# Performance work log

Hardware: AMD Instinct MI355X
Metric: run time of the kernel (lower is better)

## Reference

```python
import jax, jax.numpy as jnp
import numpy as np

B, N, D = 16, 2048, 1024
DEPTH, H, DH = 6, 16, 64
INNER = H * DH          # 1024
NL = 64                 # num latents
FF = 4 * D              # 4096
OUT = 1024


def _ln(x, g, b):
    m = jnp.mean(x, axis=-1, keepdims=True)
    v = jnp.mean((x - m) ** 2, axis=-1, keepdims=True)
    return (x - m) * jax.lax.rsqrt(v + 1e-5) * g + b


def setup_inputs() -> dict:
    key = jax.random.key(0)
    ks = jax.random.split(key, 10)
    s = lambda k, shape: (jax.random.normal(k, shape) * 0.02).astype(jnp.float32)
    return dict(
        embeds=jax.random.normal(ks[0], (B, N, D), dtype=jnp.float32),
        latents=jax.random.normal(ks[1], (NL, D), dtype=jnp.float32),
        Wq=s(ks[2], (DEPTH, D, INNER)),
        Wkv=s(ks[3], (DEPTH, D, 2 * INNER)),
        Wo=s(ks[4], (DEPTH, INNER, D)),
        W1=s(ks[5], (DEPTH, D, FF)),
        W2=s(ks[6], (DEPTH, FF, D)),
        ln_media_g=jnp.ones((DEPTH, D)), ln_media_b=jnp.zeros((DEPTH, D)),
        ln_lat_g=jnp.ones((DEPTH, D)), ln_lat_b=jnp.zeros((DEPTH, D)),
        ff_ln_g=jnp.ones((DEPTH, D)), ff_ln_b=jnp.zeros((DEPTH, D)),
        proj_W=s(ks[7], (D, OUT)),
        proj_b=jnp.zeros((OUT,)),
        final_g=jnp.ones((OUT,)), final_b=jnp.zeros((OUT,)),
        mask=jax.random.randint(ks[8], (B, N), 0, 2).astype(jnp.int32),
    )


def reference(embeds, latents, Wq, Wkv, Wo, W1, W2,
              ln_media_g, ln_media_b, ln_lat_g, ln_lat_b,
              ff_ln_g, ff_ln_b, proj_W, proj_b, final_g, final_b, mask):
    b = embeds.shape[0]
    scale = DH ** -0.5
    # cat latent mask of ones, then broadcast over (head, query) dims
    full_mask = jnp.concatenate(
        [mask.astype(embeds.dtype), jnp.ones((b, NL), embeds.dtype)], axis=1)
    keep = full_mask[:, None, None, :] > 0          # (b, 1, 1, N+NL)
    lat = jnp.broadcast_to(latents[None], (b, NL, D))
    for i in range(DEPTH):
        # --- masked cross-attention ---
        x = _ln(embeds, ln_media_g[i], ln_media_b[i])
        l = _ln(lat, ln_lat_g[i], ln_lat_b[i])
        q = (l @ Wq[i]).reshape(b, NL, H, DH).transpose(0, 2, 1, 3) * scale
        kv = jnp.concatenate([x, l], axis=1) @ Wkv[i]     # (b, N+NL, 2*inner)
        k, v = jnp.split(kv, 2, axis=-1)
        k = k.reshape(b, -1, H, DH).transpose(0, 2, 1, 3)
        v = v.reshape(b, -1, H, DH).transpose(0, 2, 1, 3)
        sim = jnp.einsum('bhid,bhjd->bhij', q, k)
        sim = sim - jax.lax.stop_gradient(jnp.max(sim, axis=-1, keepdims=True))
        sim = jnp.where(keep, sim, -10000.0)
        attn = jax.nn.softmax(sim, axis=-1)
        o = jnp.einsum('bhij,bhjd->bhid', attn, v)
        o = o.transpose(0, 2, 1, 3).reshape(b, NL, INNER)
        lat = o @ Wo[i] + lat
        # --- feed-forward ---
        h = _ln(lat, ff_ln_g[i], ff_ln_b[i])
        lat = jax.nn.gelu(h @ W1[i], approximate=False) @ W2[i] + lat
    out = lat @ proj_W + proj_b
    return _ln(out, final_g, final_b)
```

## Files before the change

kernel.cpp:

```cpp
#include <hip/hip_runtime.h>
#include <cstdint>
#include <cstddef>

typedef __bf16 bf16x8 __attribute__((ext_vector_type(8)));
typedef float f32x4 __attribute__((ext_vector_type(4)));
typedef int i32x4 __attribute__((ext_vector_type(4)));
typedef unsigned short u16;
typedef unsigned short u16x4 __attribute__((ext_vector_type(4)));

#define DEVI __device__ __forceinline__

namespace {

constexpr int kB = 16;
constexpr int kN = 2048;
constexpr int kD = 1024;
constexpr int kDepth = 6;
constexpr int kH = 16;
constexpr int kInner = 1024;
constexpr int kNL = 64;
constexpr int kFF = 4096;
constexpr int kTok = kN + kNL;

constexpr int EPI_BF16 = 0, EPI_KV_X = 1, EPI_KV_L = 2, EPI_RES = 3,
              EPI_RES_BF = 4, EPI_GELU = 5, EPI_BIAS = 6;

DEVI u16 f2bf(float f) {
  unsigned u = __builtin_bit_cast(unsigned, f);
  return (u16)((u + 0x7fffu + ((u >> 16) & 1u)) >> 16);
}
DEVI float bf2f(u16 u) { return __builtin_bit_cast(float, (unsigned)u << 16); }

__global__ __launch_bounds__(256)
void compact_k(const int* __restrict__ mask, int* __restrict__ pos,
               int* __restrict__ cnt, int* __restrict__ cpad)
{
  const int b = blockIdx.x;
  const int tid = threadIdx.x;
  __shared__ int warp_tot[4];
  const int* mb = mask + (size_t)b * kN;
  int v[8]; int loc = 0;
  #pragma unroll
  for (int j = 0; j < 8; ++j) { v[j] = (mb[tid * 8 + j] != 0); loc += v[j]; }
  int pre = loc;
  #pragma unroll
  for (int off = 1; off < 64; off <<= 1) {
    int t = __shfl_up(pre, off);
    if ((tid & 63) >= off) pre += t;
  }
  if ((tid & 63) == 63) warp_tot[tid >> 6] = pre;
  __syncthreads();
  int wbase = 0;
  for (int w = 0; w < (tid >> 6); ++w) wbase += warp_tot[w];
  const int total = warp_tot[0] + warp_tot[1] + warp_tot[2] + warp_tot[3];
  int idx = wbase + pre - loc;
  int* pb = pos + (size_t)b * kN;
  #pragma unroll
  for (int j = 0; j < 8; ++j)
    if (v[j]) pb[idx++] = tid * 8 + j;
  if (tid == 0) { cnt[b] = total; cpad[b] = (total + 127) & ~127; }
}

template<bool OBF>
__global__ __launch_bounds__(256)
void ln_k(const float* __restrict__ in, const float* __restrict__ g,
          const float* __restrict__ b, void* __restrict__ out)
{
  const int row = blockIdx.x;
  const int tid = threadIdx.x;
  const f32x4 v = *(const f32x4*)(in + (size_t)row * kD + tid * 4);
  float s = v[0] + v[1] + v[2] + v[3];
  float ss = v[0]*v[0] + v[1]*v[1] + v[2]*v[2] + v[3]*v[3];
  #pragma unroll
  for (int off = 1; off < 64; off <<= 1) {
    s += __shfl_xor(s, off);
    ss += __shfl_xor(ss, off);
  }
  __shared__ float rs[4], rss[4];
  const int wv = tid >> 6;
  if ((tid & 63) == 0) { rs[wv] = s; rss[wv] = ss; }
  __syncthreads();
  s = rs[0] + rs[1] + rs[2] + rs[3];
  ss = rss[0] + rss[1] + rss[2] + rss[3];
  const float mean = s * (1.f / kD);
  const float var = ss * (1.f / kD) - mean * mean;
  const float rstd = rsqrtf(var + 1e-5f);
  float o[4];
  #pragma unroll
  for (int j = 0; j < 4; ++j) {
    const float gv = g ? g[tid * 4 + j] : 1.f;
    const float bv = b ? b[tid * 4 + j] : 0.f;
    o[j] = (v[j] - mean) * rstd * gv + bv;
  }
  if (OBF) {
    u16x4 pk;
    #pragma unroll
    for (int j = 0; j < 4; ++j) pk[j] = f2bf(o[j]);
    ((u16x4*)out)[(size_t)row * (kD / 4) + tid] = pk;
  } else {
    f32x4 pk = {o[0], o[1], o[2], o[3]};
    ((f32x4*)out)[(size_t)row * (kD / 4) + tid] = pk;
  }
}

__global__ __launch_bounds__(256)
void ln_gather_k(const float* __restrict__ embeds, const int* __restrict__ pos,
                 const int* __restrict__ cnt, const int* __restrict__ cpad,
                 u16* __restrict__ xhat)
{
  const int b = blockIdx.y;
  const int s = blockIdx.x;
  const int tid = threadIdx.x;
  const int cv = cnt[b], cp = cpad[b];
  if (s >= cp) return;
  u16x4* dst = (u16x4*)(xhat + ((size_t)b * kN + s) * kD) + tid;
  if (s >= cv) { u16x4 z = {0, 0, 0, 0}; *dst = z; return; }
  const int row = pos[(size_t)b * kN + s];
  const f32x4 v = *(const f32x4*)(embeds + ((size_t)b * kN + row) * kD + tid * 4);
  float sm = v[0] + v[1] + v[2] + v[3];
  float ss = v[0]*v[0] + v[1]*v[1] + v[2]*v[2] + v[3]*v[3];
  #pragma unroll
  for (int off = 1; off < 64; off <<= 1) {
    sm += __shfl_xor(sm, off);
    ss += __shfl_xor(ss, off);
  }
  __shared__ float rs[4], rss[4];
  const int wv = tid >> 6;
  if ((tid & 63) == 0) { rs[wv] = sm; rss[wv] = ss; }
  __syncthreads();
  sm = rs[0] + rs[1] + rs[2] + rs[3];
  ss = rss[0] + rss[1] + rss[2] + rss[3];
  const float mean = sm * (1.f / kD);
  const float var = ss * (1.f / kD) - mean * mean;
  const float rstd = rsqrtf(var + 1e-5f);
  u16x4 pk;
  #pragma unroll
  for (int j = 0; j < 4; ++j) pk[j] = f2bf((v[j] - mean) * rstd);
  *dst = pk;
}

__global__ __launch_bounds__(256)
void transpose_cvt(const float* __restrict__ in, u16* __restrict__ out,
                   int K, int N, const float* __restrict__ gscale, float cscale)
{
  __shared__ float tile[32][33];
  const int l = blockIdx.z;
  const int n0 = blockIdx.x * 32, k0 = blockIdx.y * 32;
  const int tx = threadIdx.x & 31, ty = threadIdx.x >> 5;
  const float* src = in + (size_t)l * K * N;
  #pragma unroll
  for (int i = 0; i < 32; i += 8) {
    const int k = k0 + ty + i;
    float v = src[(size_t)k * N + n0 + tx] * cscale;
    if (gscale) v *= gscale[(size_t)l * K + k];
    tile[ty + i][tx] = v;
  }
  __syncthreads();
  u16* dst = out + (size_t)l * K * N;
  #pragma unroll
  for (int i = 0; i < 32; i += 8) {
    const int n = n0 + ty + i;
    dst[(size_t)n * K + k0 + tx] = f2bf(tile[tx][ty + i]);
  }
}

__global__ __launch_bounds__(256)
void biaskv_k(const float* __restrict__ bvec, const u16* __restrict__ WkvT,
              float* __restrict__ bias)
{
  const int l = blockIdx.y;
  const int j = blockIdx.x * 4 + (threadIdx.x >> 6);
  const int lane = threadIdx.x & 63;
  const u16* w = WkvT + ((size_t)l * 2048 + j) * kD + lane * 16;
  const float* bb = bvec + (size_t)l * kD + lane * 16;
  float acc = 0.f;
  #pragma unroll
  for (int i = 0; i < 16; ++i) acc = fmaf(bf2f(w[i]), bb[i], acc);
  #pragma unroll
  for (int off = 1; off < 64; off <<= 1) acc += __shfl_xor(acc, off);
  if (lane == 0) bias[(size_t)l * 2048 + j] = acc;
}

__global__ __launch_bounds__(256)
void lat_init_k(const float* __restrict__ latents, float* __restrict__ lat)
{
  const int idx = blockIdx.x * 256 + threadIdx.x;
  const int per = kNL * kD / 4;
  ((f32x4*)lat)[idx] = ((const f32x4*)latents)[idx & (per - 1)];
}

template<int ROWS>
DEVI void stage_tile(const u16* gbase, int ldk, char* lds, int wave, int lane) {
  constexpr int PW = ROWS / 32;
  #pragma unroll
  for (int i = 0; i < PW; ++i) {
    const int c = wave * PW + i;
    const int row = c * 8 + (lane >> 3);
    const int cb = (lane & 7) * 16;
    const int scb = cb ^ ((row & 7) << 4);
    const char* src = (const char*)(gbase + (size_t)row * ldk) + scb;
    __builtin_amdgcn_global_load_lds(
        (__attribute__((address_space(1))) void*)src,
        (__attribute__((address_space(3))) void*)(lds + c * 1024),
        16, 0, 0);
  }
}

template<int BM, int BN, int WM, int WN, int EPI>
__global__ __launch_bounds__(256, 2)
void gemm_k(const u16* __restrict__ A, const u16* __restrict__ Bt, int K, int N,
            const float* bias, const float* resid, const int* cpad,
            float* outf, u16* outb, u16* kout, u16* vtout)
{
  constexpr int WTM = BM / WM, WTN = BN / WN;
  constexpr int FM = WTM / 16, FN = WTN / 16;
  __shared__ char lds_a[BM * 128];
  __shared__ char lds_b[BN * 128];
  const int tid = threadIdx.x;
  const int wave = tid >> 6, lane = tid & 63;
  const int l15 = lane & 15, l4 = lane >> 4;
  const int wr = wave / WN, wc = wave % WN;
  const int bm = blockIdx.y * BM, bn = blockIdx.x * BN;

  if constexpr (EPI == EPI_KV_X) {
    if ((bm & (kN - 1)) >= cpad[bm >> 11]) return;
  }
  int tbase = 0;
  if constexpr (EPI == EPI_KV_L) tbase = cpad[bm >> 6];

  const u16* Ab = A + (size_t)bm * K;
  const u16* Bb = Bt + (size_t)bn * K;
  f32x4 acc[FM][FN] = {};
  for (int k0 = 0; k0 < K; k0 += 64) {
    stage_tile<BM>(Ab + k0, K, lds_a, wave, lane);
    stage_tile<BN>(Bb + k0, K, lds_b, wave, lane);
    __syncthreads();
    #pragma unroll
    for (int kk = 0; kk < 2; ++kk) {
      bf16x8 af[FM], bfr[FN];
      #pragma unroll
      for (int m = 0; m < FM; ++m) {
        const int row = wr * WTM + m * 16 + l15;
        const int cb = kk * 64 + l4 * 16;
        af[m] = *(const bf16x8*)(lds_a + row * 128 + (cb ^ ((row & 7) << 4)));
      }
      #pragma unroll
      for (int n = 0; n < FN; ++n) {
        const int row = wc * WTN + n * 16 + l15;
        const int cb = kk * 64 + l4 * 16;
        bfr[n] = *(const bf16x8*)(lds_b + row * 128 + (cb ^ ((row & 7) << 4)));
      }
      #pragma unroll
      for (int m = 0; m < FM; ++m)
        #pragma unroll
        for (int n = 0; n < FN; ++n)
          acc[m][n] = __builtin_amdgcn_mfma_f32_16x16x32_bf16(af[m], bfr[n], acc[m][n], 0, 0, 0);
    }
    __syncthreads();
  }
  #pragma unroll
  for (int m = 0; m < FM; ++m) {
    #pragma unroll
    for (int n = 0; n < FN; ++n) {
      const int r = bm + wr * WTM + m * 16 + l4 * 4;
      const int c = bn + wc * WTN + n * 16 + l15;
      f32x4 v = acc[m][n];
      if constexpr (EPI == EPI_BF16) {
        #pragma unroll
        for (int j = 0; j < 4; ++j) outb[(size_t)(r + j) * N + c] = f2bf(v[j]);
      } else if constexpr (EPI == EPI_GELU) {
        #pragma unroll
        for (int j = 0; j < 4; ++j) {
          const float x = v[j];
          outb[(size_t)(r + j) * N + c] = f2bf(0.5f * x * (1.f + erff(x * 0.7071067811865475f)));
        }
      } else if constexpr (EPI == EPI_RES || EPI == EPI_RES_BF) {
        #pragma unroll
        for (int j = 0; j < 4; ++j) {
          const float x = v[j] + resid[(size_t)(r + j) * N + c];
          outf[(size_t)(r + j) * N + c] = x;
          if constexpr (EPI == EPI_RES_BF) outb[(size_t)(r + j) * N + c] = f2bf(x);
        }
      } else if constexpr (EPI == EPI_BIAS) {
        #pragma unroll
        for (int j = 0; j < 4; ++j) outf[(size_t)(r + j) * N + c] = v[j] + bias[c];
      } else {
        int bb, t;
        float bv = 0.f;
        if constexpr (EPI == EPI_KV_X) { bb = r >> 11; t = r & (kN - 1); bv = bias[c]; }
        else                           { bb = r >> 6;  t = tbase + (r & 63); }
        if (c < kInner) {
          #pragma unroll
          for (int j = 0; j < 4; ++j)
            kout[((size_t)bb * kTok + t + j) * kInner + c] = f2bf(v[j] + bv);
        } else {
          u16x4 pk;
          #pragma unroll
          for (int j = 0; j < 4; ++j) pk[j] = f2bf(v[j] + bv);
          *(u16x4*)(vtout + ((size_t)bb * kInner + (c - kInner)) * kTok + t) = pk;
        }
      }
    }
  }
}

__global__ __launch_bounds__(256)
void attn_k(const u16* __restrict__ Kb, const u16* __restrict__ VT,
            const u16* __restrict__ Q, const int* __restrict__ cnt,
            const int* __restrict__ cpad, u16* __restrict__ O)
{
  const int bh = blockIdx.x;
  const int b = bh >> 4, h = bh & 15;
  const int tid = threadIdx.x;
  const int wave = tid >> 6, lane = tid & 63;
  const int l15 = lane & 15, l4 = lane >> 4;
  const int cv = cnt[b], cp = cpad[b];
  const int nt = (cp >> 6) + 1;

  __shared__ char p_lds[4][64 * 128];
  __shared__ float o_sm[64 * 65];
  __shared__ float red_m[4][64], red_l[4][64], lstar[64];

  bf16x8 qf[4][2];
  #pragma unroll
  for (int n = 0; n < 4; ++n)
    #pragma unroll
    for (int kk = 0; kk < 2; ++kk)
      qf[n][kk] = *(const bf16x8*)(Q + (size_t)(b * kNL + n * 16 + l15) * kInner + h * 64 + kk * 32 + 8 * l4);

  f32x4 oacc[4][4] = {};
  float mst[4], lst[4];
  #pragma unroll
  for (int n = 0; n < 4; ++n) { mst[n] = -1e30f; lst[n] = 0.f; }

  char* pw = p_lds[wave];

  for (int t = wave; t < nt; t += 4) {
    const int key0 = t * 64;
    const bool isLat = (t == nt - 1);
    f32x4 s[4][4] = {};
    #pragma unroll
    for (int kk = 0; kk < 2; ++kk) {
      bf16x8 kf[4];
      #pragma unroll
      for (int m = 0; m < 4; ++m)
        kf[m] = *(const bf16x8*)(Kb + ((size_t)b * kTok + key0 + m * 16 + l15) * kInner + h * 64 + kk * 32 + 8 * l4);
      #pragma unroll
      for (int m = 0; m < 4; ++m)
        #pragma unroll
        for (int n = 0; n < 4; ++n)
          s[m][n] = __builtin_amdgcn_mfma_f32_16x16x32_bf16(kf[m], qf[n][kk], s[m][n], 0, 0, 0);
    }
    const bool allv = isLat || (key0 + 64 <= cv);
    bool vld[4][4];
    #pragma unroll
    for (int m = 0; m < 4; ++m)
      #pragma unroll
      for (int j = 0; j < 4; ++j)
        vld[m][j] = allv || (key0 + m * 16 + l4 * 4 + j < cv);
    #pragma unroll
    for (int n = 0; n < 4; ++n) {
      float tm = -1e30f;
      #pragma unroll
      for (int m = 0; m < 4; ++m)
        #pragma unroll
        for (int j = 0; j < 4; ++j)
          tm = fmaxf(tm, vld[m][j] ? s[m][n][j] : -1e30f);
      tm = fmaxf(tm, __shfl_xor(tm, 16));
      tm = fmaxf(tm, __shfl_xor(tm, 32));
      const float mnew = fmaxf(mst[n], tm);
      const float sc = __expf(mst[n] - mnew);
      mst[n] = mnew;
      float rsum = 0.f;
      #pragma unroll
      for (int m = 0; m < 4; ++m)
        #pragma unroll
        for (int j = 0; j < 4; ++j) {
          const float pv = vld[m][j] ? __expf(s[m][n][j] - mnew) : 0.f;
          s[m][n][j] = pv;
          rsum += pv;
        }
      rsum += __shfl_xor(rsum, 16);
      rsum += __shfl_xor(rsum, 32);
      lst[n] = lst[n] * sc + rsum;
      #pragma unroll
      for (int m = 0; m < 4; ++m) oacc[m][n] *= sc;
    }
    #pragma unroll
    for (int m = 0; m < 4; ++m)
      #pragma unroll
      for (int n = 0; n < 4; ++n) {
        const int q = n * 16 + l15;
        const int kb = (m * 16 + l4 * 4) * 2;
        u16x4 pk;
        #pragma unroll
        for (int j = 0; j < 4; ++j) pk[j] = f2bf(s[m][n][j]);
        *(u16x4*)(pw + q * 128 + (kb ^ ((q & 7) << 4))) = pk;
      }
    #pragma unroll
    for (int kk = 0; kk < 2; ++kk) {
      bf16x8 vf[4], pf[4];
      #pragma unroll
      for (int m = 0; m < 4; ++m)
        vf[m] = *(const bf16x8*)(VT + ((size_t)b * kInner + h * 64 + m * 16 + l15) * kTok + key0 + kk * 32 + 8 * l4);
      #pragma unroll
      for (int n = 0; n < 4; ++n) {
        const int q = n * 16 + l15;
        const int cb = kk * 64 + l4 * 16;
        pf[n] = *(const bf16x8*)(pw + q * 128 + (cb ^ ((q & 7) << 4)));
      }
      #pragma unroll
      for (int m = 0; m < 4; ++m)
        #pragma unroll
        for (int n = 0; n < 4; ++n)
          oacc[m][n] = __builtin_amdgcn_mfma_f32_16x16x32_bf16(vf[m], pf[n], oacc[m][n], 0, 0, 0);
    }
  }

  if (l4 == 0) {
    #pragma unroll
    for (int n = 0; n < 4; ++n) {
      red_m[wave][n * 16 + l15] = mst[n];
      red_l[wave][n * 16 + l15] = lst[n];
    }
  }
  __syncthreads();
  float coef[4];
  #pragma unroll
  for (int n = 0; n < 4; ++n) {
    const int q = n * 16 + l15;
    const float m0 = red_m[0][q], m1 = red_m[1][q], m2 = red_m[2][q], m3 = red_m[3][q];
    const float msx = fmaxf(fmaxf(m0, m1), fmaxf(m2, m3));
    coef[n] = __expf(mst[n] - msx);
    if (wave == 0 && l4 == 0)
      lstar[q] = red_l[0][q] * __expf(m0 - msx) + red_l[1][q] * __expf(m1 - msx)
               + red_l[2][q] * __expf(m2 - msx) + red_l[3][q] * __expf(m3 - msx);
  }
  #pragma unroll
  for (int m = 0; m < 4; ++m)
    #pragma unroll
    for (int n = 0; n < 4; ++n)
      oacc[m][n] *= coef[n];
  for (int w = 0; w < 4; ++w) {
    if (wave == w) {
      #pragma unroll
      for (int m = 0; m < 4; ++m)
        #pragma unroll
        for (int n = 0; n < 4; ++n) {
          const int q = n * 16 + l15;
          #pragma unroll
          for (int j = 0; j < 4; ++j) {
            const int dh = m * 16 + l4 * 4 + j;
            if (w == 0) o_sm[q * 65 + dh] = oacc[m][n][j];
            else        o_sm[q * 65 + dh] += oacc[m][n][j];
          }
        }
    }
    __syncthreads();
  }
  for (int i = tid; i < 64 * 64; i += 256) {
    const int q = i >> 6, dh = i & 63;
    O[(size_t)(b * kNL + q) * kInner + h * 64 + dh] = f2bf(o_sm[q * 65 + dh] / lstar[q]);
  }
}

}

extern "C" void kernel_launch(void* const* d_in, const int* in_sizes, int n_in,
                              void* d_out, int out_size, void* d_ws, size_t ws_size,
                              hipStream_t stream)
{
  (void)in_sizes; (void)n_in; (void)out_size; (void)ws_size;
  const float* embeds  = (const float*)d_in[0];
  const float* latents = (const float*)d_in[1];
  const float* Wq    = (const float*)d_in[2];
  const float* Wkv   = (const float*)d_in[3];
  const float* Wo    = (const float*)d_in[4];
  const float* W1    = (const float*)d_in[5];
  const float* W2    = (const float*)d_in[6];
  const float* lmg   = (const float*)d_in[7];
  const float* lmb   = (const float*)d_in[8];
  const float* llg   = (const float*)d_in[9];
  const float* llb   = (const float*)d_in[10];
  const float* ffg   = (const float*)d_in[11];
  const float* ffbv  = (const float*)d_in[12];
  const float* projW = (const float*)d_in[13];
  const float* projB = (const float*)d_in[14];
  const float* fing  = (const float*)d_in[15];
  const float* finb  = (const float*)d_in[16];
  const int*   mask  = (const int*)d_in[17];
  float* out = (float*)d_out;

  char* p = (char*)d_ws;
  auto alloc = [&](size_t bytes) -> char* {
    char* r = p; p += (bytes + 255) & ~(size_t)255; return r;
  };
  u16* WqT   = (u16*)alloc((size_t)kDepth * kInner * kD * 2);
  u16* WkvT  = (u16*)alloc((size_t)kDepth * 2048 * kD * 2);
  u16* WkvfT = (u16*)alloc((size_t)kDepth * 2048 * kD * 2);
  u16* WoT   = (u16*)alloc((size_t)kDepth * kD * kInner * 2);
  u16* W1T   = (u16*)alloc((size_t)kDepth * kFF * kD * 2);
  u16* W2T   = (u16*)alloc((size_t)kDepth * kD * kFF * 2);
  u16* projT = (u16*)alloc((size_t)kD * kD * 2);
  float* bkv = (float*)alloc((size_t)kDepth * 2048 * 4);
  u16* xhat  = (u16*)alloc((size_t)kB * kN * kD * 2);
  u16* Kb    = (u16*)alloc((size_t)kB * kTok * kInner * 2);
  u16* VTb   = (u16*)alloc((size_t)kB * kInner * kTok * 2);
  u16* qb    = (u16*)alloc((size_t)kB * kNL * kInner * 2);
  u16* lln   = (u16*)alloc((size_t)kB * kNL * kD * 2);
  u16* ob    = (u16*)alloc((size_t)kB * kNL * kInner * 2);
  float* lat = (float*)alloc((size_t)kB * kNL * kD * 4);
  u16* latb  = (u16*)alloc((size_t)kB * kNL * kD * 2);
  u16* hb    = (u16*)alloc((size_t)kB * kNL * kD * 2);
  u16* ffbuf = (u16*)alloc((size_t)kB * kNL * kFF * 2);
  float* tmpo = (float*)alloc((size_t)kB * kNL * kD * 4);
  int* pos  = (int*)alloc((size_t)kB * kN * 4);
  int* cnt  = (int*)alloc(kB * 4);
  int* cpad = (int*)alloc(kB * 4);

  const dim3 blk(256);

  compact_k<<<dim3(kB), blk, 0, stream>>>(mask, pos, cnt, cpad);
  transpose_cvt<<<dim3(kInner/32, kD/32, kDepth), blk, 0, stream>>>(Wq, WqT, kD, kInner, nullptr, 0.125f);
  transpose_cvt<<<dim3(2048/32, kD/32, kDepth), blk, 0, stream>>>(Wkv, WkvT, kD, 2048, nullptr, 1.f);
  transpose_cvt<<<dim3(2048/32, kD/32, kDepth), blk, 0, stream>>>(Wkv, WkvfT, kD, 2048, lmg, 1.f);
  transpose_cvt<<<dim3(kD/32, kInner/32, kDepth), blk, 0, stream>>>(Wo, WoT, kInner, kD, nullptr, 1.f);
  transpose_cvt<<<dim3(kFF/32, kD/32, kDepth), blk, 0, stream>>>(W1, W1T, kD, kFF, nullptr, 1.f);
  transpose_cvt<<<dim3(kD/32, kFF/32, kDepth), blk, 0, stream>>>(W2, W2T, kFF, kD, nullptr, 1.f);
  transpose_cvt<<<dim3(kD/32, kD/32, 1), blk, 0, stream>>>(projW, projT, kD, kD, nullptr, 1.f);
  biaskv_k<<<dim3(512, kDepth), blk, 0, stream>>>(lmb, WkvT, bkv);
  ln_gather_k<<<dim3(kN, kB), blk, 0, stream>>>(embeds, pos, cnt, cpad, xhat);
  lat_init_k<<<dim3(kB * kNL * kD / 4 / 256), blk, 0, stream>>>(latents, lat);

  for (int i = 0; i < kDepth; ++i) {
    const u16* WqTi   = WqT   + (size_t)i * kInner * kD;
    const u16* WkvTi  = WkvT  + (size_t)i * 2048 * kD;
    const u16* WkvfTi = WkvfT + (size_t)i * 2048 * kD;
    const u16* WoTi   = WoT   + (size_t)i * kD * kInner;
    const u16* W1Ti   = W1T   + (size_t)i * kFF * kD;
    const u16* W2Ti   = W2T   + (size_t)i * kD * kFF;
    const float* bkvi = bkv   + (size_t)i * 2048;

    ln_k<true><<<dim3(kB * kNL), blk, 0, stream>>>(lat, llg + i * kD, llb + i * kD, lln);
    gemm_k<64,64,2,2,EPI_BF16><<<dim3(kInner/64, kB*kNL/64), blk, 0, stream>>>(
        lln, WqTi, kD, kInner, nullptr, nullptr, nullptr, nullptr, qb, nullptr, nullptr);
    gemm_k<64,64,2,2,EPI_KV_L><<<dim3(2048/64, kB*kNL/64), blk, 0, stream>>>(
        lln, WkvTi, kD, 2048, nullptr, nullptr, cpad, nullptr, nullptr, Kb, VTb);
    gemm_k<128,128,2,2,EPI_KV_X><<<dim3(2048/128, kB*kN/128), blk, 0, stream>>>(
        xhat, WkvfTi, kD, 2048, bkvi, nullptr, cpad, nullptr, nullptr, Kb, VTb);
    attn_k<<<dim3(kB * kH), blk, 0, stream>>>(Kb, VTb, qb, cnt, cpad, ob);
    gemm_k<64,64,2,2,EPI_RES><<<dim3(kD/64, kB*kNL/64), blk, 0, stream>>>(
        ob, WoTi, kInner, kD, nullptr, lat, nullptr, lat, nullptr, nullptr, nullptr);
    ln_k<true><<<dim3(kB * kNL), blk, 0, stream>>>(lat, ffg + i * kD, ffbv + i * kD, hb);
    gemm_k<64,64,2,2,EPI_GELU><<<dim3(kFF/64, kB*kNL/64), blk, 0, stream>>>(
        hb, W1Ti, kD, kFF, nullptr, nullptr, nullptr, nullptr, ffbuf, nullptr, nullptr);
    gemm_k<64,64,2,2,EPI_RES_BF><<<dim3(kD/64, kB*kNL/64), blk, 0, stream>>>(
        ffbuf, W2Ti, kFF, kD, nullptr, lat, nullptr, lat, latb, nullptr, nullptr);
  }
  gemm_k<64,64,2,2,EPI_BIAS><<<dim3(kD/64, kB*kNL/64), blk, 0, stream>>>(
      latb, projT, kD, kD, projB, nullptr, nullptr, tmpo, nullptr, nullptr, nullptr);
  ln_k<false><<<dim3(kB * kNL), blk, 0, stream>>>(tmpo, fing, finb, out);
}
```

Measured before the change: 2.060 ms.

## Fuse Q and latent KV GEMMs and stage transposed V writes through LDS

Concatenates the transposed Wq and Wkv weights into one Wqkv matrix so the latent-side Q and KV projections run as a single GEMM launch, and merges the two Wkv transposes into one kernel that writes both the plain and gamma-folded copies. In the large media KV GEMM, the V-transpose epilogue now goes through an XOR-swizzled LDS tile so each thread issues 16-byte row stores along tokens instead of scattered 8-byte ones. This reduces launches and uncoalesced global writes, at the cost of an extra LDS pass and a barrier in the epilogue.

```diff
diff --git a/kernel.cpp b/kernel.cpp
--- a/kernel.cpp
+++ b/kernel.cpp
@@ -4,9 +4,9 @@
 
 typedef __bf16 bf16x8 __attribute__((ext_vector_type(8)));
 typedef float f32x4 __attribute__((ext_vector_type(4)));
-typedef int i32x4 __attribute__((ext_vector_type(4)));
 typedef unsigned short u16;
 typedef unsigned short u16x4 __attribute__((ext_vector_type(4)));
+typedef unsigned short u16x8 __attribute__((ext_vector_type(8)));
 
 #define DEVI __device__ __forceinline__
 
@@ -22,8 +22,8 @@
 constexpr int kFF = 4096;
 constexpr int kTok = kN + kNL;
 
-constexpr int EPI_BF16 = 0, EPI_KV_X = 1, EPI_KV_L = 2, EPI_RES = 3,
-              EPI_RES_BF = 4, EPI_GELU = 5, EPI_BIAS = 6;
+constexpr int EPI_KV_X = 1, EPI_RES = 3, EPI_RES_BF = 4, EPI_GELU = 5,
+              EPI_BIAS = 6, EPI_QKV = 7;
 
 DEVI u16 f2bf(float f) {
   unsigned u = __builtin_bit_cast(unsigned, f);
@@ -141,7 +141,7 @@
 
 __global__ __launch_bounds__(256)
 void transpose_cvt(const float* __restrict__ in, u16* __restrict__ out,
-                   int K, int N, const float* __restrict__ gscale, float cscale)
+                   int K, int N, size_t ldo, int coff, float cscale)
 {
   __shared__ float tile[32][33];
   const int l = blockIdx.z;
@@ -149,29 +149,50 @@
   const int tx = threadIdx.x & 31, ty = threadIdx.x >> 5;
   const float* src = in + (size_t)l * K * N;
   #pragma unroll
-  for (int i = 0; i < 32; i += 8) {
-    const int k = k0 + ty + i;
-    float v = src[(size_t)k * N + n0 + tx] * cscale;
-    if (gscale) v *= gscale[(size_t)l * K + k];
-    tile[ty + i][tx] = v;
-  }
+  for (int i = 0; i < 32; i += 8)
+    tile[ty + i][tx] = src[(size_t)(k0 + ty + i) * N + n0 + tx] * cscale;
   __syncthreads();
-  u16* dst = out + (size_t)l * K * N;
+  u16* dst = out + (size_t)l * ldo;
   #pragma unroll
   for (int i = 0; i < 32; i += 8) {
     const int n = n0 + ty + i;
-    dst[(size_t)n * K + k0 + tx] = f2bf(tile[tx][ty + i]);
-  }
-}
-
-__global__ __launch_bounds__(256)
-void biaskv_k(const float* __restrict__ bvec, const u16* __restrict__ WkvT,
+    dst[(size_t)(coff + n) * K + k0 + tx] = f2bf(tile[tx][ty + i]);
+  }
+}
+
+__global__ __launch_bounds__(256)
+void transpose_kv(const float* __restrict__ in, u16* __restrict__ out_plain,
+                  u16* __restrict__ out_fold, const float* __restrict__ gvec)
+{
+  __shared__ float tile[32][33];
+  const int l = blockIdx.z;
+  const int n0 = blockIdx.x * 32, k0 = blockIdx.y * 32;
+  const int tx = threadIdx.x & 31, ty = threadIdx.x >> 5;
+  const float* src = in + (size_t)l * kD * 2048;
+  #pragma unroll
+  for (int i = 0; i < 32; i += 8)
+    tile[ty + i][tx] = src[(size_t)(k0 + ty + i) * 2048 + n0 + tx];
+  __syncthreads();
+  const float gv = gvec[(size_t)l * kD + k0 + tx];
+  u16* dp = out_plain + (size_t)l * (3072 * kD);
+  u16* df = out_fold + (size_t)l * (2048 * kD);
+  #pragma unroll
+  for (int i = 0; i < 32; i += 8) {
+    const int n = n0 + ty + i;
+    const float v = tile[tx][ty + i];
+    dp[(size_t)(1024 + n) * kD + k0 + tx] = f2bf(v);
+    df[(size_t)n * kD + k0 + tx] = f2bf(v * gv);
+  }
+}
+
+__global__ __launch_bounds__(256)
+void biaskv_k(const float* __restrict__ bvec, const u16* __restrict__ WqkvT,
               float* __restrict__ bias)
 {
   const int l = blockIdx.y;
   const int j = blockIdx.x * 4 + (threadIdx.x >> 6);
   const int lane = threadIdx.x & 63;
-  const u16* w = WkvT + ((size_t)l * 2048 + j) * kD + lane * 16;
+  const u16* w = WqkvT + (size_t)l * (3072 * kD) + (size_t)(1024 + j) * kD + lane * 16;
   const float* bb = bvec + (size_t)l * kD + lane * 16;
   float acc = 0.f;
   #pragma unroll
@@ -214,8 +235,9 @@
 {
   constexpr int WTM = BM / WM, WTN = BN / WN;
   constexpr int FM = WTM / 16, FN = WTN / 16;
-  __shared__ char lds_a[BM * 128];
-  __shared__ char lds_b[BN * 128];
+  __shared__ char lds_raw[(BM + BN) * 128];
+  char* lds_a = lds_raw;
+  char* lds_b = lds_raw + BM * 128;
   const int tid = threadIdx.x;
   const int wave = tid >> 6, lane = tid & 63;
   const int l15 = lane & 15, l4 = lane >> 4;
@@ -226,7 +248,7 @@
     if ((bm & (kN - 1)) >= cpad[bm >> 11]) return;
   }
   int tbase = 0;
-  if constexpr (EPI == EPI_KV_L) tbase = cpad[bm >> 6];
+  if constexpr (EPI == EPI_QKV) tbase = cpad[bm >> 6];
 
   const u16* Ab = A + (size_t)bm * K;
   const u16* Bb = Bt + (size_t)bn * K;
@@ -258,6 +280,47 @@
     }
     __syncthreads();
   }
+
+  if constexpr (EPI == EPI_KV_X) {
+    const int bb = bm >> 11;
+    const int tloc = bm & (kN - 1);
+    if (bn >= kInner) {
+      #pragma unroll
+      for (int m = 0; m < FM; ++m)
+        #pragma unroll
+        for (int n = 0; n < FN; ++n) {
+          const int rl = wr * WTM + m * 16 + l4 * 4;
+          const int cl = wc * WTN + n * 16 + l15;
+          const float bv = bias[bn + cl];
+          u16x4 pk;
+          #pragma unroll
+          for (int j = 0; j < 4; ++j) pk[j] = f2bf(acc[m][n][j] + bv);
+          *(u16x4*)(lds_raw + cl * 256 + ((rl * 2) ^ ((cl & 15) << 4))) = pk;
+        }
+      __syncthreads();
+      #pragma unroll
+      for (int it = 0; it < 8; ++it) {
+        const int idx = it * 256 + tid;
+        const int cl = idx >> 4, ch = idx & 15;
+        const u16x8 val = *(const u16x8*)(lds_raw + cl * 256 + ((ch * 16) ^ ((cl & 15) << 4)));
+        *(u16x8*)(vtout + ((size_t)bb * kInner + (bn - kInner) + cl) * kTok + tloc + ch * 8) = val;
+      }
+    } else {
+      #pragma unroll
+      for (int m = 0; m < FM; ++m)
+        #pragma unroll
+        for (int n = 0; n < FN; ++n) {
+          const int t = tloc + wr * WTM + m * 16 + l4 * 4;
+          const int c = bn + wc * WTN + n * 16 + l15;
+          const float bv = bias[c];
+          #pragma unroll
+          for (int j = 0; j < 4; ++j)
+            kout[((size_t)bb * kTok + t + j) * kInner + c] = f2bf(acc[m][n][j] + bv);
+        }
+    }
+    return;
+  }
+
   #pragma unroll
   for (int m = 0; m < FM; ++m) {
     #pragma unroll
@@ -265,10 +328,7 @@
       const int r = bm + wr * WTM + m * 16 + l4 * 4;
       const int c = bn + wc * WTN + n * 16 + l15;
       f32x4 v = acc[m][n];
-      if constexpr (EPI == EPI_BF16) {
-        #pragma unroll
-        for (int j = 0; j < 4; ++j) outb[(size_t)(r + j) * N + c] = f2bf(v[j]);
-      } else if constexpr (EPI == EPI_GELU) {
+      if constexpr (EPI == EPI_GELU) {
         #pragma unroll
         for (int j = 0; j < 4; ++j) {
           const float x = v[j];
@@ -284,20 +344,20 @@
       } else if constexpr (EPI == EPI_BIAS) {
         #pragma unroll
         for (int j = 0; j < 4; ++j) outf[(size_t)(r + j) * N + c] = v[j] + bias[c];
-      } else {
-        int bb, t;
-        float bv = 0.f;
-        if constexpr (EPI == EPI_KV_X) { bb = r >> 11; t = r & (kN - 1); bv = bias[c]; }
-        else                           { bb = r >> 6;  t = tbase + (r & 63); }
-        if (c < kInner) {
+      } else if constexpr (EPI == EPI_QKV) {
+        const int bb = r >> 6;
+        if (c < 1024) {
+          #pragma unroll
+          for (int j = 0; j < 4; ++j) outb[(size_t)(r + j) * kInner + c] = f2bf(v[j]);
+        } else if (c < 2048) {
           #pragma unroll
           for (int j = 0; j < 4; ++j)
-            kout[((size_t)bb * kTok + t + j) * kInner + c] = f2bf(v[j] + bv);
+            kout[((size_t)bb * kTok + tbase + (r & 63) + j) * kInner + (c - 1024)] = f2bf(v[j]);
         } else {
           u16x4 pk;
           #pragma unroll
-          for (int j = 0; j < 4; ++j) pk[j] = f2bf(v[j] + bv);
-          *(u16x4*)(vtout + ((size_t)bb * kInner + (c - kInner)) * kTok + t) = pk;
+          for (int j = 0; j < 4; ++j) pk[j] = f2bf(v[j]);
+          *(u16x4*)(vtout + ((size_t)bb * kInner + (c - 2048)) * kTok + tbase + (r & 63)) = pk;
         }
       }
     }
@@ -495,8 +555,7 @@
   auto alloc = [&](size_t bytes) -> char* {
     char* r = p; p += (bytes + 255) & ~(size_t)255; return r;
   };
-  u16* WqT   = (u16*)alloc((size_t)kDepth * kInner * kD * 2);
-  u16* WkvT  = (u16*)alloc((size_t)kDepth * 2048 * kD * 2);
+  u16* WqkvT = (u16*)alloc((size_t)kDepth * 3072 * kD * 2);
   u16* WkvfT = (u16*)alloc((size_t)kDepth * 2048 * kD * 2);
   u16* WoT   = (u16*)alloc((size_t)kDepth * kD * kInner * 2);
   u16* W1T   = (u16*)alloc((size_t)kDepth * kFF * kD * 2);
@@ -521,20 +580,18 @@
   const dim3 blk(256);
 
   compact_k<<<dim3(kB), blk, 0, stream>>>(mask, pos, cnt, cpad);
-  transpose_cvt<<<dim3(kInner/32, kD/32, kDepth), blk, 0, stream>>>(Wq, WqT, kD, kInner, nullptr, 0.125f);
-  transpose_cvt<<<dim3(2048/32, kD/32, kDepth), blk, 0, stream>>>(Wkv, WkvT, kD, 2048, nullptr, 1.f);
-  transpose_cvt<<<dim3(2048/32, kD/32, kDepth), blk, 0, stream>>>(Wkv, WkvfT, kD, 2048, lmg, 1.f);
-  transpose_cvt<<<dim3(kD/32, kInner/32, kDepth), blk, 0, stream>>>(Wo, WoT, kInner, kD, nullptr, 1.f);
-  transpose_cvt<<<dim3(kFF/32, kD/32, kDepth), blk, 0, stream>>>(W1, W1T, kD, kFF, nullptr, 1.f);
-  transpose_cvt<<<dim3(kD/32, kFF/32, kDepth), blk, 0, stream>>>(W2, W2T, kFF, kD, nullptr, 1.f);
-  transpose_cvt<<<dim3(kD/32, kD/32, 1), blk, 0, stream>>>(projW, projT, kD, kD, nullptr, 1.f);
-  biaskv_k<<<dim3(512, kDepth), blk, 0, stream>>>(lmb, WkvT, bkv);
+  transpose_cvt<<<dim3(kInner/32, kD/32, kDepth), blk, 0, stream>>>(Wq, WqkvT, kD, kInner, (size_t)3072 * kD, 0, 0.125f);
+  transpose_kv<<<dim3(2048/32, kD/32, kDepth), blk, 0, stream>>>(Wkv, WqkvT, WkvfT, lmg);
+  transpose_cvt<<<dim3(kD/32, kInner/32, kDepth), blk, 0, stream>>>(Wo, WoT, kInner, kD, (size_t)kD * kInner, 0, 1.f);
+  transpose_cvt<<<dim3(kFF/32, kD/32, kDepth), blk, 0, stream>>>(W1, W1T, kD, kFF, (size_t)kFF * kD, 0, 1.f);
+  transpose_cvt<<<dim3(kD/32, kFF/32, kDepth), blk, 0, stream>>>(W2, W2T, kFF, kD, (size_t)kD * kFF, 0, 1.f);
+  transpose_cvt<<<dim3(kD/32, kD/32, 1), blk, 0, stream>>>(projW, projT, kD, kD, (size_t)kD * kD, 0, 1.f);
+  biaskv_k<<<dim3(512, kDepth), blk, 0, stream>>>(lmb, WqkvT, bkv);
   ln_gather_k<<<dim3(kN, kB), blk, 0, stream>>>(embeds, pos, cnt, cpad, xhat);
   lat_init_k<<<dim3(kB * kNL * kD / 4 / 256), blk, 0, stream>>>(latents, lat);
 
   for (int i = 0; i < kDepth; ++i) {
-    const u16* WqTi   = WqT   + (size_t)i * kInner * kD;
-    const u16* WkvTi  = WkvT  + (size_t)i * 2048 * kD;
+    const u16* WqkvTi = WqkvT + (size_t)i * 3072 * kD;
     const u16* WkvfTi = WkvfT + (size_t)i * 2048 * kD;
     const u16* WoTi   = WoT   + (size_t)i * kD * kInner;
     const u16* W1Ti   = W1T   + (size_t)i * kFF * kD;
@@ -542,10 +599,8 @@
     const float* bkvi = bkv   + (size_t)i * 2048;
 
     ln_k<true><<<dim3(kB * kNL), blk, 0, stream>>>(lat, llg + i * kD, llb + i * kD, lln);
-    gemm_k<64,64,2,2,EPI_BF16><<<dim3(kInner/64, kB*kNL/64), blk, 0, stream>>>(
-        lln, WqTi, kD, kInner, nullptr, nullptr, nullptr, nullptr, qb, nullptr, nullptr);
-    gemm_k<64,64,2,2,EPI_KV_L><<<dim3(2048/64, kB*kNL/64), blk, 0, stream>>>(
-        lln, WkvTi, kD, 2048, nullptr, nullptr, cpad, nullptr, nullptr, Kb, VTb);
+    gemm_k<64,64,2,2,EPI_QKV><<<dim3(3072/64, kB*kNL/64), blk, 0, stream>>>(
+        lln, WqkvTi, kD, 3072, nullptr, nullptr, cpad, nullptr, qb, Kb, VTb);
     gemm_k<128,128,2,2,EPI_KV_X><<<dim3(2048/128, kB*kN/128), blk, 0, stream>>>(
         xhat, WkvfTi, kD, 2048, bkvi, nullptr, cpad, nullptr, nullptr, Kb, VTb);
     attn_k<<<dim3(kB * kH), blk, 0, stream>>>(Kb, VTb, qb, cnt, cpad, ob);
```

New measurement: 1.812 ms. -12.0%, faster.
